# Kernel tuning notes

Measured on AMD Instinct MI355X. Metric: run time of the kernel, lower is better.

## Reference

```python
import jax, jax.numpy as jnp
import numpy as np

B, C, H, W = 4, 256, 64, 64
NUM_HEADS, HIDDEN = 2, 64


def setup_inputs() -> dict:
    key = jax.random.key(0)
    k1, k2, k3 = jax.random.split(key, 3)
    x = jax.random.normal(k1, (B, C, H, W), dtype=jnp.float32)
    # per-head fused QKV 1x1 conv weights: [num_heads, 3*hidden, C]
    embed_w = jax.random.normal(k2, (NUM_HEADS, 3 * HIDDEN, C), dtype=jnp.float32) * (2.0 / C) ** 0.5
    embed_b = jnp.zeros((NUM_HEADS, 3 * HIDDEN), dtype=jnp.float32)
    # output ConvTranspose2d kernel-1 weight: [in=hidden*heads, out=C]
    out_w = jax.random.normal(k3, (HIDDEN * NUM_HEADS, C), dtype=jnp.float32) * (2.0 / C) ** 0.5
    out_b = jnp.zeros((C,), dtype=jnp.float32)
    return {"x": x, "embed_w": embed_w, "embed_b": embed_b, "out_w": out_w, "out_b": out_b}


def reference(x, embed_w, embed_b, out_w, out_b):
    b, c, h, w = x.shape
    n = h * w
    scale = c ** (-0.5)  # scaled=True uses in_channels**-0.5
    xf = x.reshape(b, c, n)  # [B,C,N]
    # fused QKV projection for all heads (1x1 conv == channel matmul)
    qkv = jnp.einsum('bcn,hdc->bhdn', xf, embed_w) + embed_b[None, :, :, None]  # [B,Hh,3*hc,N]
    q, k, v = jnp.split(qkv, 3, axis=2)  # each [B,Hh,hc,N]
    # attention over flattened spatial positions
    attn = jax.nn.softmax(jnp.einsum('bhcm,bhcn->bhmn', q, k) * scale, axis=-1)  # [B,Hh,N,N]
    o = jnp.einsum('bhmn,bhcn->bhcm', attn, v)  # [B,Hh,hc,N]
    o = o.reshape(b, -1, n)  # concat heads -> [B, hc*Hh, N]
    # output 1x1 transpose conv: sum over input channel dim d of weight[d, c]
    out = jnp.einsum('bdn,dc->bcn', o, out_w) + out_b[None, :, None]
    out = out.reshape(b, c, h, w)
    return out + x  # residual=True
```

## Files before the change

kernel.cpp:

```cpp
#include <hip/hip_runtime.h>

#define B_SZ  4
#define C_IN  256
#define N_POS 4096
#define NH    2
#define HC    64

typedef __attribute__((ext_vector_type(8))) __bf16 bf16x8;
typedef __attribute__((ext_vector_type(4))) float  f32x4;
typedef unsigned short u16;

__device__ __forceinline__ u16 f2bf(float f) {
  unsigned u = __float_as_uint(f);
  u = u + 0x7FFF + ((u >> 16) & 1);
  return (u16)(u >> 16);
}

#if __has_builtin(__builtin_amdgcn_exp2f)
  #define EXP2(x) __builtin_amdgcn_exp2f(x)
#else
  #define EXP2(x) exp2f(x)
#endif

__device__ __forceinline__ unsigned cvtpk_bf16(float lo, float hi) {
  unsigned r;
  asm("v_cvt_pk_bf16_f32 %0, %1, %2" : "=v"(r) : "v"(lo), "v"(hi));
  return r;
}

__device__ __forceinline__ void gload_lds16(const void* g, void* l) {
  __builtin_amdgcn_global_load_lds(
      (const __attribute__((address_space(1))) unsigned*)g,
      (__attribute__((address_space(3))) unsigned*)l, 16, 0, 0);
}

__global__ __launch_bounds__(256) void k_prep_x(const float* __restrict__ x,
                                                u16* __restrict__ xt) {
  __shared__ float tile[32][33];
  int b = blockIdx.z, c0 = blockIdx.y * 32, n0 = blockIdx.x * 32;
  int tx = threadIdx.x, ty = threadIdx.y;
  const float* src = x + ((size_t)b * C_IN + c0) * N_POS + n0;
#pragma unroll
  for (int i = 0; i < 4; i++) tile[ty + 8*i][tx] = src[(size_t)(ty + 8*i) * N_POS + tx];
  __syncthreads();
  u16* dst = xt + ((size_t)b * N_POS + n0) * C_IN + c0;
#pragma unroll
  for (int i = 0; i < 4; i++) dst[(size_t)(ty + 8*i) * C_IN + tx] = f2bf(tile[tx][ty + 8*i]);
}

__global__ __launch_bounds__(256) void k_prep_w(const float* __restrict__ ew,
                                                const float* __restrict__ ow,
                                                u16* __restrict__ wbf,
                                                u16* __restrict__ w2t) {
  int i = blockIdx.x * 256 + threadIdx.x;
  if (i < 384 * 256) wbf[i] = f2bf(ew[i]);
  if (i < 128 * 256) {
    int d = i >> 8, c = i & 255;
    w2t[c * 128 + d] = f2bf(ow[i]);
  }
}

__global__ __launch_bounds__(256) void k_qkv(const u16* __restrict__ xt,
                                             const u16* __restrict__ wbf,
                                             const float* __restrict__ eb,
                                             u16* __restrict__ Qt,
                                             u16* __restrict__ Kt,
                                             u16* __restrict__ Vs) {
  int b = blockIdx.z;
  int mt = blockIdx.y;
  int nt = blockIdx.x;
  int w = threadIdx.x >> 6, l = threadIdx.x & 63;
  int lr = l & 15, lg = l >> 4;
  int h = mt / 3, type = mt % 3;

  const u16* arow = xt + ((size_t)b * N_POS + nt*64 + w*16 + lr) * C_IN + lg*8;
  const u16* brow = wbf + ((size_t)(mt*64) + lr) * C_IN + lg*8;

  f32x4 acc[4] = {};
#pragma unroll
  for (int kk = 0; kk < 8; kk++) {
    bf16x8 a = *(const bf16x8*)(arow + kk*32);
#pragma unroll
    for (int mf = 0; mf < 4; mf++) {
      bf16x8 bf = *(const bf16x8*)(brow + (size_t)mf*16*C_IN + kk*32);
      acc[mf] = __builtin_amdgcn_mfma_f32_16x16x32_bf16(a, bf, acc[mf], 0, 0, 0);
    }
  }

  const float QSCALE = 0.0625f * 1.44269504088896f;
  int bh = b * NH + h;
  int n0 = nt*64 + w*16 + lg*4;
#pragma unroll
  for (int mf = 0; mf < 4; mf++) {
    int cl = mf*16 + lr;
    float bias = eb[h*192 + type*64 + cl];
    if (type == 0) {
      u16* q = Qt + (size_t)bh * N_POS * HC;
#pragma unroll
      for (int r = 0; r < 4; r++) q[(size_t)(n0+r)*HC + cl] = f2bf((acc[mf][r] + bias) * QSCALE);
    } else if (type == 1) {
      u16* kd = Kt + (size_t)bh * N_POS * HC;
#pragma unroll
      for (int r = 0; r < 4; r++) kd[(size_t)(n0+r)*HC + cl] = f2bf(acc[mf][r] + bias);
    } else {
      u16* vd = Vs + (size_t)bh * (N_POS * HC);
      size_t idx = ((((size_t)nt*2 + (w>>1))*4 + lg)*64 + cl)*8 + 4*(w&1);
      ushort4 pk;
      pk.x = f2bf(acc[mf][0] + bias);
      pk.y = f2bf(acc[mf][1] + bias);
      pk.z = f2bf(acc[mf][2] + bias);
      pk.w = f2bf(acc[mf][3] + bias);
      *(ushort4*)(vd + idx) = pk;
    }
  }
}

__device__ __forceinline__ void softmax_tile(f32x4 (&s)[4], f32x4& psv, float& rm,
                                             f32x4 (&o)[4]) {
  float mx = s[0][0];
#pragma unroll
  for (int nf = 0; nf < 4; nf++)
#pragma unroll
    for (int r = 0; r < 4; r++) mx = fmaxf(mx, s[nf][r]);
  mx = fmaxf(mx, __shfl_xor(mx, 16));
  mx = fmaxf(mx, __shfl_xor(mx, 32));
  float nm = fmaxf(rm, mx);
  float corr = EXP2(rm - nm);
  rm = nm;
#pragma unroll
  for (int r = 0; r < 4; r++) psv[r] *= corr;
#pragma unroll
  for (int nf = 0; nf < 4; nf++)
#pragma unroll
    for (int r = 0; r < 4; r++) {
      float p = EXP2(s[nf][r] - nm);
      s[nf][r] = p;
      psv[r] += p;
    }
#pragma unroll
  for (int cf = 0; cf < 4; cf++)
#pragma unroll
    for (int r = 0; r < 4; r++) o[cf][r] *= corr;
}

__global__ __launch_bounds__(1024, 4) void k_attn(const u16* __restrict__ Qt,
                                                  const u16* __restrict__ Kt,
                                                  const u16* __restrict__ Vs,
                                                  u16* __restrict__ Ot) {
  int id = blockIdx.x;
  int bh = id & 7;
  int mt = id >> 3;
  int b = bh >> 1, h = bh & 1;
  int tid = threadIdx.x;
  int wid = tid >> 6;
  int l = tid & 63, lr = l & 15, lg = l >> 4;
  int qi = wid & 3;
  int ci = wid >> 2;
  int m0 = mt*128 + qi*32;

  __shared__ __align__(16) char smem[131072];
  __shared__ float Lps[4][8][16];
  __shared__ float Lm[4][8][16];

  bf16x8 qf[2][2];
#pragma unroll
  for (int sub = 0; sub < 2; sub++) {
    const u16* qb = Qt + ((size_t)bh * N_POS + m0 + sub*16 + lr) * HC + lg*8;
    qf[sub][0] = *(const bf16x8*)qb;
    qf[sub][1] = *(const bf16x8*)(qb + 32);
  }

  const char* Kt_bh = (const char*)(Kt + (size_t)bh * N_POS * HC);
  const char* Vs_bh = (const char*)(Vs + (size_t)bh * N_POS * HC);
  int gtid = tid & 255;

  f32x4 o0[4] = {}, o1[4] = {};
  f32x4 ps0 = {}, ps1 = {};
  float rm0 = -1e30f, rm1 = -1e30f;
  int xr = (lr & 7) << 4;

  union PF { bf16x8 v; unsigned u[4]; };

  auto stage = [&](int tile, char* sb) {
    const char* ksrc = Kt_bh + (size_t)tile * 8192;
    const char* vsrc = Vs_bh + (size_t)tile * 8192;
#pragma unroll
    for (int j = 0; j < 2; j++) {
      int off = (j*256 + gtid) * 16;
      int koff = off ^ (((off >> 7) & 7) << 4);
      gload_lds16(ksrc + koff, sb + off);
      gload_lds16(vsrc + off, sb + 8192 + off);
    }
  };

  stage(ci*16, smem + ci*16384);
  __syncthreads();

  int buf = 0;
  for (int t = 0; t < 16; t++) {
    if (t < 15) stage(ci*16 + t + 1, smem + (buf^1)*65536 + ci*16384);

    const char* Kb = smem + buf*65536 + ci*16384;
    const char* Vb = Kb + 8192;

    f32x4 s0[4], s1[4];
#pragma unroll
    for (int nf = 0; nf < 4; nf++) {
      const char* kr = Kb + (nf*16 + lr) * 128;
      bf16x8 k0 = *(const bf16x8*)(kr + ((lg*16)      ^ xr));
      bf16x8 k1 = *(const bf16x8*)(kr + ((lg*16 + 64) ^ xr));
      f32x4 z0 = {}, z1 = {};
      z0 = __builtin_amdgcn_mfma_f32_16x16x32_bf16(k0, qf[0][0], z0, 0, 0, 0);
      s0[nf] = __builtin_amdgcn_mfma_f32_16x16x32_bf16(k1, qf[0][1], z0, 0, 0, 0);
      z1 = __builtin_amdgcn_mfma_f32_16x16x32_bf16(k0, qf[1][0], z1, 0, 0, 0);
      s1[nf] = __builtin_amdgcn_mfma_f32_16x16x32_bf16(k1, qf[1][1], z1, 0, 0, 0);
    }

    softmax_tile(s0, ps0, rm0, o0);
    softmax_tile(s1, ps1, rm1, o1);

#pragma unroll
    for (int kk = 0; kk < 2; kk++) {
      PF pa, pb;
      pa.u[0] = cvtpk_bf16(s0[2*kk+0][0], s0[2*kk+0][1]);
      pa.u[1] = cvtpk_bf16(s0[2*kk+0][2], s0[2*kk+0][3]);
      pa.u[2] = cvtpk_bf16(s0[2*kk+1][0], s0[2*kk+1][1]);
      pa.u[3] = cvtpk_bf16(s0[2*kk+1][2], s0[2*kk+1][3]);
      pb.u[0] = cvtpk_bf16(s1[2*kk+0][0], s1[2*kk+0][1]);
      pb.u[1] = cvtpk_bf16(s1[2*kk+0][2], s1[2*kk+0][3]);
      pb.u[2] = cvtpk_bf16(s1[2*kk+1][0], s1[2*kk+1][1]);
      pb.u[3] = cvtpk_bf16(s1[2*kk+1][2], s1[2*kk+1][3]);
#pragma unroll
      for (int cf = 0; cf < 4; cf++) {
        bf16x8 vf = *(const bf16x8*)(Vb + (kk*4 + lg)*1024 + (cf*16 + lr)*16);
        o0[cf] = __builtin_amdgcn_mfma_f32_16x16x32_bf16(vf, pa.v, o0[cf], 0, 0, 0);
        o1[cf] = __builtin_amdgcn_mfma_f32_16x16x32_bf16(vf, pb.v, o1[cf], 0, 0, 0);
      }
    }

    __syncthreads();
    buf ^= 1;
  }

  float psa = ps0[0] + ps0[1] + ps0[2] + ps0[3];
  psa += __shfl_xor(psa, 16);
  psa += __shfl_xor(psa, 32);
  float psb = ps1[0] + ps1[1] + ps1[2] + ps1[3];
  psb += __shfl_xor(psb, 16);
  psb += __shfl_xor(psb, 32);

  float (*Lo)[8][16][64] = (float (*)[8][16][64])smem;
#pragma unroll
  for (int cf = 0; cf < 4; cf++) {
    *(f32x4*)&Lo[ci][qi*2+0][lr][cf*16 + 4*lg] = o0[cf];
    *(f32x4*)&Lo[ci][qi*2+1][lr][cf*16 + 4*lg] = o1[cf];
  }
  if (lg == 0) {
    Lps[ci][qi*2+0][lr] = psa; Lm[ci][qi*2+0][lr] = rm0;
    Lps[ci][qi*2+1][lr] = psb; Lm[ci][qi*2+1][lr] = rm1;
  }
  __syncthreads();

  int row = tid >> 3;
  int c0 = (tid & 7) * 8;
  int g = row >> 4, r2 = row & 15;
  float m0_ = Lm[0][g][r2], m1_ = Lm[1][g][r2];
  float m2_ = Lm[2][g][r2], m3_ = Lm[3][g][r2];
  float M = fmaxf(fmaxf(m0_, m1_), fmaxf(m2_, m3_));
  float w0 = EXP2(m0_ - M), w1 = EXP2(m1_ - M);
  float w2 = EXP2(m2_ - M), w3 = EXP2(m3_ - M);
  f32x4 accA, accB;
  {
    f32x4 a0 = *(const f32x4*)&Lo[0][g][r2][c0];
    f32x4 a1 = *(const f32x4*)&Lo[1][g][r2][c0];
    f32x4 a2 = *(const f32x4*)&Lo[2][g][r2][c0];
    f32x4 a3 = *(const f32x4*)&Lo[3][g][r2][c0];
#pragma unroll
    for (int i = 0; i < 4; i++) accA[i] = a0[i]*w0 + a1[i]*w1 + a2[i]*w2 + a3[i]*w3;
    f32x4 b0 = *(const f32x4*)&Lo[0][g][r2][c0+4];
    f32x4 b1 = *(const f32x4*)&Lo[1][g][r2][c0+4];
    f32x4 b2 = *(const f32x4*)&Lo[2][g][r2][c0+4];
    f32x4 b3 = *(const f32x4*)&Lo[3][g][r2][c0+4];
#pragma unroll
    for (int i = 0; i < 4; i++) accB[i] = b0[i]*w0 + b1[i]*w1 + b2[i]*w2 + b3[i]*w3;
  }
  float pst = Lps[0][g][r2]*w0 + Lps[1][g][r2]*w1
            + Lps[2][g][r2]*w2 + Lps[3][g][r2]*w3;
  float rinv = 1.0f / pst;
  u16* ob = Ot + ((size_t)b * N_POS + mt*128 + row) * (NH*HC) + h*HC + c0;
  uint4 st;
  st.x = cvtpk_bf16(accA[0]*rinv, accA[1]*rinv);
  st.y = cvtpk_bf16(accA[2]*rinv, accA[3]*rinv);
  st.z = cvtpk_bf16(accB[0]*rinv, accB[1]*rinv);
  st.w = cvtpk_bf16(accB[2]*rinv, accB[3]*rinv);
  *(uint4*)ob = st;
}

__global__ __launch_bounds__(256) void k_out(const u16* __restrict__ Ot,
                                             const u16* __restrict__ w2t,
                                             const float* __restrict__ obias,
                                             const float* __restrict__ x,
                                             float* __restrict__ out) {
  int b = blockIdx.z;
  int ct = blockIdx.y;
  int nt = blockIdx.x;
  int w = threadIdx.x >> 6, l = threadIdx.x & 63;
  int lr = l & 15, lg = l >> 4;

  const u16* arow = Ot + ((size_t)b * N_POS + nt*64 + w*16 + lr) * 128 + lg*8;
  const u16* brow = w2t + ((size_t)(ct*64) + lr) * 128 + lg*8;

  f32x4 acc[4] = {};
#pragma unroll
  for (int kk = 0; kk < 4; kk++) {
    bf16x8 a = *(const bf16x8*)(arow + kk*32);
#pragma unroll
    for (int cf = 0; cf < 4; cf++) {
      bf16x8 bf = *(const bf16x8*)(brow + (size_t)cf*16*128 + kk*32);
      acc[cf] = __builtin_amdgcn_mfma_f32_16x16x32_bf16(a, bf, acc[cf], 0, 0, 0);
    }
  }

  int n0 = nt*64 + w*16 + lg*4;
#pragma unroll
  for (int cf = 0; cf < 4; cf++) {
    int c = ct*64 + cf*16 + lr;
    float bias = obias[c];
    const float* xp = x + ((size_t)b * C_IN + c) * N_POS + n0;
    float* op = out + ((size_t)b * C_IN + c) * N_POS + n0;
    f32x4 xv = *(const f32x4*)xp;
    f32x4 rv;
#pragma unroll
    for (int i = 0; i < 4; i++) rv[i] = acc[cf][i] + bias + xv[i];
    *(f32x4*)op = rv;
  }
}

extern "C" void kernel_launch(void* const* d_in, const int* in_sizes, int n_in,
                              void* d_out, int out_size, void* d_ws, size_t ws_size,
                              hipStream_t stream) {
  const float* x  = (const float*)d_in[0];
  const float* ew = (const float*)d_in[1];
  const float* eb = (const float*)d_in[2];
  const float* ow = (const float*)d_in[3];
  const float* ob = (const float*)d_in[4];
  float* out = (float*)d_out;

  char* ws = (char*)d_ws;
  u16* xt  = (u16*)(ws + 0);
  u16* wbf = (u16*)(ws + 8388608);
  u16* w2t = (u16*)(ws + 8585216);
  u16* Qt  = (u16*)(ws + 8650752);
  u16* Kt  = (u16*)(ws + 12845056);
  u16* Vs  = (u16*)(ws + 17039360);
  u16* Ot  = (u16*)(ws + 21233664);

  hipLaunchKernelGGL(k_prep_x, dim3(128, 8, 4), dim3(32, 8), 0, stream, x, xt);
  hipLaunchKernelGGL(k_prep_w, dim3(384), dim3(256), 0, stream, ew, ow, wbf, w2t);
  hipLaunchKernelGGL(k_qkv,  dim3(64, 6, 4), dim3(256), 0, stream, xt, wbf, eb, Qt, Kt, Vs);
  hipLaunchKernelGGL(k_attn, dim3(256),      dim3(1024), 0, stream, Qt, Kt, Vs, Ot);
  hipLaunchKernelGGL(k_out,  dim3(64, 4, 4), dim3(256), 0, stream, Ot, w2t, ob, x, out);
}
```

Measured before the change: 105.9 us.

## Halve attention block size, single-buffer KV, swizzle LDS reduction, remap QKV grid

The attention kernel drops from 1024-thread blocks covering 128 query rows to 512-thread blocks covering 64 rows, and launches twice as many blocks. K/V staging becomes single-buffered with an extra barrier, which halves LDS per block so more blocks can share a CU, but loads no longer overlap compute within a block. MFMA sections are wrapped in s_setprio. The cross-wave reduction buffer gets a rotated column layout to avoid LDS bank conflicts. The QKV projection uses a 1D grid whose low bits pick (batch, head) so that work is spread across XCDs.

```diff
diff --git a/kernel.cpp b/kernel.cpp
--- a/kernel.cpp
+++ b/kernel.cpp
@@ -66,12 +66,16 @@
                                              u16* __restrict__ Qt,
                                              u16* __restrict__ Kt,
                                              u16* __restrict__ Vs) {
-  int b = blockIdx.z;
-  int mt = blockIdx.y;
-  int nt = blockIdx.x;
+  int id = blockIdx.x;
+  int xcd = id & 7;
+  int b = xcd >> 1, half = xcd & 1;
+  int rest = id >> 3;
+  int type = rest % 3;
+  int nt = rest / 3;
+  int mt = half*3 + type;
+  int h = half;
   int w = threadIdx.x >> 6, l = threadIdx.x & 63;
   int lr = l & 15, lg = l >> 4;
-  int h = mt / 3, type = mt % 3;
 
   const u16* arow = xt + ((size_t)b * N_POS + nt*64 + w*16 + lr) * C_IN + lg*8;
   const u16* brow = wbf + ((size_t)(mt*64) + lr) * C_IN + lg*8;
@@ -143,10 +147,10 @@
     for (int r = 0; r < 4; r++) o[cf][r] *= corr;
 }
 
-__global__ __launch_bounds__(1024, 4) void k_attn(const u16* __restrict__ Qt,
-                                                  const u16* __restrict__ Kt,
-                                                  const u16* __restrict__ Vs,
-                                                  u16* __restrict__ Ot) {
+__global__ __launch_bounds__(512, 4) void k_attn(const u16* __restrict__ Qt,
+                                                 const u16* __restrict__ Kt,
+                                                 const u16* __restrict__ Vs,
+                                                 u16* __restrict__ Ot) {
   int id = blockIdx.x;
   int bh = id & 7;
   int mt = id >> 3;
@@ -154,13 +158,13 @@
   int tid = threadIdx.x;
   int wid = tid >> 6;
   int l = tid & 63, lr = l & 15, lg = l >> 4;
-  int qi = wid & 3;
-  int ci = wid >> 2;
-  int m0 = mt*128 + qi*32;
-
-  __shared__ __align__(16) char smem[131072];
-  __shared__ float Lps[4][8][16];
-  __shared__ float Lm[4][8][16];
+  int qi = wid & 1;
+  int ci = wid >> 1;
+  int m0 = mt*64 + qi*32;
+
+  __shared__ __align__(16) char smem[65536];
+  __shared__ float Lps[4][4][16];
+  __shared__ float Lm[4][4][16];
 
   bf16x8 qf[2][2];
 #pragma unroll
@@ -172,7 +176,7 @@
 
   const char* Kt_bh = (const char*)(Kt + (size_t)bh * N_POS * HC);
   const char* Vs_bh = (const char*)(Vs + (size_t)bh * N_POS * HC);
-  int gtid = tid & 255;
+  int gtid = tid & 127;
 
   f32x4 o0[4] = {}, o1[4] = {};
   f32x4 ps0 = {}, ps1 = {};
@@ -181,29 +185,28 @@
 
   union PF { bf16x8 v; unsigned u[4]; };
 
-  auto stage = [&](int tile, char* sb) {
+  auto stage = [&](int tile) {
     const char* ksrc = Kt_bh + (size_t)tile * 8192;
     const char* vsrc = Vs_bh + (size_t)tile * 8192;
-#pragma unroll
-    for (int j = 0; j < 2; j++) {
-      int off = (j*256 + gtid) * 16;
+    char* sb = smem + ci*16384;
+#pragma unroll
+    for (int j = 0; j < 4; j++) {
+      int off = (j*128 + gtid) * 16;
       int koff = off ^ (((off >> 7) & 7) << 4);
       gload_lds16(ksrc + koff, sb + off);
       gload_lds16(vsrc + off, sb + 8192 + off);
     }
   };
 
-  stage(ci*16, smem + ci*16384);
+  stage(ci*16);
   __syncthreads();
 
-  int buf = 0;
   for (int t = 0; t < 16; t++) {
-    if (t < 15) stage(ci*16 + t + 1, smem + (buf^1)*65536 + ci*16384);
-
-    const char* Kb = smem + buf*65536 + ci*16384;
+    const char* Kb = smem + ci*16384;
     const char* Vb = Kb + 8192;
 
     f32x4 s0[4], s1[4];
+    __builtin_amdgcn_s_setprio(1);
 #pragma unroll
     for (int nf = 0; nf < 4; nf++) {
       const char* kr = Kb + (nf*16 + lr) * 128;
@@ -215,10 +218,12 @@
       z1 = __builtin_amdgcn_mfma_f32_16x16x32_bf16(k0, qf[1][0], z1, 0, 0, 0);
       s1[nf] = __builtin_amdgcn_mfma_f32_16x16x32_bf16(k1, qf[1][1], z1, 0, 0, 0);
     }
+    __builtin_amdgcn_s_setprio(0);
 
     softmax_tile(s0, ps0, rm0, o0);
     softmax_tile(s1, ps1, rm1, o1);
 
+    __builtin_amdgcn_s_setprio(1);
 #pragma unroll
     for (int kk = 0; kk < 2; kk++) {
       PF pa, pb;
@@ -237,9 +242,11 @@
         o1[cf] = __builtin_amdgcn_mfma_f32_16x16x32_bf16(vf, pb.v, o1[cf], 0, 0, 0);
       }
     }
+    __builtin_amdgcn_s_setprio(0);
 
     __syncthreads();
-    buf ^= 1;
+    if (t < 15) stage(ci*16 + t + 1);
+    __syncthreads();
   }
 
   float psa = ps0[0] + ps0[1] + ps0[2] + ps0[3];
@@ -249,11 +256,12 @@
   psb += __shfl_xor(psb, 16);
   psb += __shfl_xor(psb, 32);
 
-  float (*Lo)[8][16][64] = (float (*)[8][16][64])smem;
+  float (*Lo)[4][16][64] = (float (*)[4][16][64])smem;
 #pragma unroll
   for (int cf = 0; cf < 4; cf++) {
-    *(f32x4*)&Lo[ci][qi*2+0][lr][cf*16 + 4*lg] = o0[cf];
-    *(f32x4*)&Lo[ci][qi*2+1][lr][cf*16 + 4*lg] = o1[cf];
+    int colw = ((cf*16 + 4*lg) + 4*lr) & 63;
+    *(f32x4*)&Lo[ci][qi*2+0][lr][colw] = o0[cf];
+    *(f32x4*)&Lo[ci][qi*2+1][lr][colw] = o1[cf];
   }
   if (lg == 0) {
     Lps[ci][qi*2+0][lr] = psa; Lm[ci][qi*2+0][lr] = rm0;
@@ -269,25 +277,27 @@
   float M = fmaxf(fmaxf(m0_, m1_), fmaxf(m2_, m3_));
   float w0 = EXP2(m0_ - M), w1 = EXP2(m1_ - M);
   float w2 = EXP2(m2_ - M), w3 = EXP2(m3_ - M);
+  int ca = (c0 + 4*r2) & 63;
+  int cb = (c0 + 4 + 4*r2) & 63;
   f32x4 accA, accB;
   {
-    f32x4 a0 = *(const f32x4*)&Lo[0][g][r2][c0];
-    f32x4 a1 = *(const f32x4*)&Lo[1][g][r2][c0];
-    f32x4 a2 = *(const f32x4*)&Lo[2][g][r2][c0];
-    f32x4 a3 = *(const f32x4*)&Lo[3][g][r2][c0];
+    f32x4 a0 = *(const f32x4*)&Lo[0][g][r2][ca];
+    f32x4 a1 = *(const f32x4*)&Lo[1][g][r2][ca];
+    f32x4 a2 = *(const f32x4*)&Lo[2][g][r2][ca];
+    f32x4 a3 = *(const f32x4*)&Lo[3][g][r2][ca];
 #pragma unroll
     for (int i = 0; i < 4; i++) accA[i] = a0[i]*w0 + a1[i]*w1 + a2[i]*w2 + a3[i]*w3;
-    f32x4 b0 = *(const f32x4*)&Lo[0][g][r2][c0+4];
-    f32x4 b1 = *(const f32x4*)&Lo[1][g][r2][c0+4];
-    f32x4 b2 = *(const f32x4*)&Lo[2][g][r2][c0+4];
-    f32x4 b3 = *(const f32x4*)&Lo[3][g][r2][c0+4];
+    f32x4 b0 = *(const f32x4*)&Lo[0][g][r2][cb];
+    f32x4 b1 = *(const f32x4*)&Lo[1][g][r2][cb];
+    f32x4 b2 = *(const f32x4*)&Lo[2][g][r2][cb];
+    f32x4 b3 = *(const f32x4*)&Lo[3][g][r2][cb];
 #pragma unroll
     for (int i = 0; i < 4; i++) accB[i] = b0[i]*w0 + b1[i]*w1 + b2[i]*w2 + b3[i]*w3;
   }
   float pst = Lps[0][g][r2]*w0 + Lps[1][g][r2]*w1
             + Lps[2][g][r2]*w2 + Lps[3][g][r2]*w3;
   float rinv = 1.0f / pst;
-  u16* ob = Ot + ((size_t)b * N_POS + mt*128 + row) * (NH*HC) + h*HC + c0;
+  u16* ob = Ot + ((size_t)b * N_POS + mt*64 + row) * (NH*HC) + h*HC + c0;
   uint4 st;
   st.x = cvtpk_bf16(accA[0]*rinv, accA[1]*rinv);
   st.y = cvtpk_bf16(accA[2]*rinv, accA[3]*rinv);
@@ -357,7 +367,7 @@
 
   hipLaunchKernelGGL(k_prep_x, dim3(128, 8, 4), dim3(32, 8), 0, stream, x, xt);
   hipLaunchKernelGGL(k_prep_w, dim3(384), dim3(256), 0, stream, ew, ow, wbf, w2t);
-  hipLaunchKernelGGL(k_qkv,  dim3(64, 6, 4), dim3(256), 0, stream, xt, wbf, eb, Qt, Kt, Vs);
-  hipLaunchKernelGGL(k_attn, dim3(256),      dim3(1024), 0, stream, Qt, Kt, Vs, Ot);
+  hipLaunchKernelGGL(k_qkv,  dim3(1536),     dim3(256), 0, stream, xt, wbf, eb, Qt, Kt, Vs);
+  hipLaunchKernelGGL(k_attn, dim3(512),      dim3(512), 0, stream, Qt, Kt, Vs, Ot);
   hipLaunchKernelGGL(k_out,  dim3(64, 4, 4), dim3(256), 0, stream, Ot, w2t, ob, x, out);
 }
```

Measured after the change: 107.2 us. About the same (+1.2%).

## Fuse x transpose/bf16 cast into QKV GEMM, add MFMA priority and LDS swizzle

Applied to the files above, without the earlier changes.

Removes the separate k_prep_x kernel. The QKV kernel now loads fp32 x directly, converts it to bf16 and stages a swizzled 64x256 tile in LDS. Each block computes all 192 output channels of one head for 64 positions, so x is read once per head instead of once per Q/K/V type. This drops a kernel launch and the round trip of the intermediate xt buffer, at the cost of 32KB of LDS per block and more accumulators per thread. The attention kernel also raises wave priority around its MFMA sections and rotates columns in the output-merge LDS buffer to reduce bank conflicts.

```diff
diff --git a/kernel.cpp b/kernel.cpp
--- a/kernel.cpp
+++ b/kernel.cpp
@@ -32,20 +32,6 @@
   __builtin_amdgcn_global_load_lds(
       (const __attribute__((address_space(1))) unsigned*)g,
       (__attribute__((address_space(3))) unsigned*)l, 16, 0, 0);
-}
-
-__global__ __launch_bounds__(256) void k_prep_x(const float* __restrict__ x,
-                                                u16* __restrict__ xt) {
-  __shared__ float tile[32][33];
-  int b = blockIdx.z, c0 = blockIdx.y * 32, n0 = blockIdx.x * 32;
-  int tx = threadIdx.x, ty = threadIdx.y;
-  const float* src = x + ((size_t)b * C_IN + c0) * N_POS + n0;
-#pragma unroll
-  for (int i = 0; i < 4; i++) tile[ty + 8*i][tx] = src[(size_t)(ty + 8*i) * N_POS + tx];
-  __syncthreads();
-  u16* dst = xt + ((size_t)b * N_POS + n0) * C_IN + c0;
-#pragma unroll
-  for (int i = 0; i < 4; i++) dst[(size_t)(ty + 8*i) * C_IN + tx] = f2bf(tile[tx][ty + 8*i]);
 }
 
 __global__ __launch_bounds__(256) void k_prep_w(const float* __restrict__ ew,
@@ -60,57 +46,91 @@
   }
 }
 
-__global__ __launch_bounds__(256) void k_qkv(const u16* __restrict__ xt,
+__global__ __launch_bounds__(256) void k_qkv(const float* __restrict__ x,
                                              const u16* __restrict__ wbf,
                                              const float* __restrict__ eb,
                                              u16* __restrict__ Qt,
                                              u16* __restrict__ Kt,
                                              u16* __restrict__ Vs) {
-  int b = blockIdx.z;
-  int mt = blockIdx.y;
-  int nt = blockIdx.x;
-  int w = threadIdx.x >> 6, l = threadIdx.x & 63;
-  int lr = l & 15, lg = l >> 4;
-  int h = mt / 3, type = mt % 3;
-
-  const u16* arow = xt + ((size_t)b * N_POS + nt*64 + w*16 + lr) * C_IN + lg*8;
-  const u16* brow = wbf + ((size_t)(mt*64) + lr) * C_IN + lg*8;
-
-  f32x4 acc[4] = {};
+  int id = blockIdx.x;
+  int xcd = id & 7;
+  int b = xcd >> 1, h = xcd & 1;
+  int nt = id >> 3;
+  int tid = threadIdx.x;
+  int w = tid >> 6, l = tid & 63, lr = l & 15, lg = l >> 4;
+
+  __shared__ __align__(16) u16 Xl[64 * 256];
+
+  const float* xb = x + (size_t)b * C_IN * N_POS + nt*64;
+  {
+    int n = l;
+#pragma unroll
+    for (int pass = 0; pass < 8; pass++) {
+      int oct = w + pass*4;
+      int cb8 = oct * 8;
+      float v[8];
+#pragma unroll
+      for (int j = 0; j < 8; j++) v[j] = xb[(size_t)(cb8 + j) * N_POS + n];
+      union { bf16x8 vv; unsigned u[4]; } pk;
+#pragma unroll
+      for (int jj = 0; jj < 4; jj++) pk.u[jj] = cvtpk_bf16(v[2*jj], v[2*jj+1]);
+      int slot = oct ^ ((n & 7) << 2);
+      *(bf16x8*)&Xl[n * 256 + slot * 8] = pk.vv;
+    }
+  }
+  __syncthreads();
+
+  f32x4 acc[4][3] = {};
+  const u16* brow[3];
+#pragma unroll
+  for (int i = 0; i < 3; i++)
+    brow[i] = wbf + (size_t)(h*192 + (3*w + i)*16 + lr) * C_IN + lg*8;
+
 #pragma unroll
   for (int kk = 0; kk < 8; kk++) {
-    bf16x8 a = *(const bf16x8*)(arow + kk*32);
-#pragma unroll
-    for (int mf = 0; mf < 4; mf++) {
-      bf16x8 bf = *(const bf16x8*)(brow + (size_t)mf*16*C_IN + kk*32);
-      acc[mf] = __builtin_amdgcn_mfma_f32_16x16x32_bf16(a, bf, acc[mf], 0, 0, 0);
+    bf16x8 bfr[3];
+#pragma unroll
+    for (int i = 0; i < 3; i++) bfr[i] = *(const bf16x8*)(brow[i] + kk*32);
+#pragma unroll
+    for (int nsub = 0; nsub < 4; nsub++) {
+      int n2 = nsub*16 + lr;
+      int sp = (kk*4 + lg) ^ ((lr & 7) << 2);
+      bf16x8 a = *(const bf16x8*)&Xl[n2*256 + sp*8];
+#pragma unroll
+      for (int i = 0; i < 3; i++)
+        acc[nsub][i] = __builtin_amdgcn_mfma_f32_16x16x32_bf16(a, bfr[i], acc[nsub][i], 0, 0, 0);
     }
   }
 
   const float QSCALE = 0.0625f * 1.44269504088896f;
   int bh = b * NH + h;
-  int n0 = nt*64 + w*16 + lg*4;
-#pragma unroll
-  for (int mf = 0; mf < 4; mf++) {
+#pragma unroll
+  for (int i = 0; i < 3; i++) {
+    int s3 = 3*w + i;
+    int type = s3 >> 2, mf = s3 & 3;
     int cl = mf*16 + lr;
     float bias = eb[h*192 + type*64 + cl];
-    if (type == 0) {
-      u16* q = Qt + (size_t)bh * N_POS * HC;
-#pragma unroll
-      for (int r = 0; r < 4; r++) q[(size_t)(n0+r)*HC + cl] = f2bf((acc[mf][r] + bias) * QSCALE);
-    } else if (type == 1) {
-      u16* kd = Kt + (size_t)bh * N_POS * HC;
-#pragma unroll
-      for (int r = 0; r < 4; r++) kd[(size_t)(n0+r)*HC + cl] = f2bf(acc[mf][r] + bias);
-    } else {
-      u16* vd = Vs + (size_t)bh * (N_POS * HC);
-      size_t idx = ((((size_t)nt*2 + (w>>1))*4 + lg)*64 + cl)*8 + 4*(w&1);
-      ushort4 pk;
-      pk.x = f2bf(acc[mf][0] + bias);
-      pk.y = f2bf(acc[mf][1] + bias);
-      pk.z = f2bf(acc[mf][2] + bias);
-      pk.w = f2bf(acc[mf][3] + bias);
-      *(ushort4*)(vd + idx) = pk;
+#pragma unroll
+    for (int nsub = 0; nsub < 4; nsub++) {
+      int n0 = nt*64 + nsub*16 + lg*4;
+      if (type == 0) {
+        u16* q = Qt + (size_t)bh * N_POS * HC;
+#pragma unroll
+        for (int r = 0; r < 4; r++) q[(size_t)(n0+r)*HC + cl] = f2bf((acc[nsub][i][r] + bias) * QSCALE);
+      } else if (type == 1) {
+        u16* kd = Kt + (size_t)bh * N_POS * HC;
+#pragma unroll
+        for (int r = 0; r < 4; r++) kd[(size_t)(n0+r)*HC + cl] = f2bf(acc[nsub][i][r] + bias);
+      } else {
+        u16* vd = Vs + (size_t)bh * (N_POS * HC);
+        size_t idx = ((((size_t)nt*2 + (nsub>>1))*4 + lg)*64 + cl)*8 + 4*(nsub&1);
+        ushort4 pk;
+        pk.x = f2bf(acc[nsub][i][0] + bias);
+        pk.y = f2bf(acc[nsub][i][1] + bias);
+        pk.z = f2bf(acc[nsub][i][2] + bias);
+        pk.w = f2bf(acc[nsub][i][3] + bias);
+        *(ushort4*)(vd + idx) = pk;
+      }
     }
   }
 }
@@ -204,6 +224,7 @@
     const char* Vb = Kb + 8192;
 
     f32x4 s0[4], s1[4];
+    __builtin_amdgcn_s_setprio(1);
 #pragma unroll
     for (int nf = 0; nf < 4; nf++) {
       const char* kr = Kb + (nf*16 + lr) * 128;
@@ -215,10 +236,12 @@
       z1 = __builtin_amdgcn_mfma_f32_16x16x32_bf16(k0, qf[1][0], z1, 0, 0, 0);
       s1[nf] = __builtin_amdgcn_mfma_f32_16x16x32_bf16(k1, qf[1][1], z1, 0, 0, 0);
     }
+    __builtin_amdgcn_s_setprio(0);
 
     softmax_tile(s0, ps0, rm0, o0);
     softmax_tile(s1, ps1, rm1, o1);
 
+    __builtin_amdgcn_s_setprio(1);
 #pragma unroll
     for (int kk = 0; kk < 2; kk++) {
       PF pa, pb;
@@ -237,6 +260,7 @@
         o1[cf] = __builtin_amdgcn_mfma_f32_16x16x32_bf16(vf, pb.v, o1[cf], 0, 0, 0);
       }
     }
+    __builtin_amdgcn_s_setprio(0);
 
     __syncthreads();
     buf ^= 1;
@@ -252,8 +276,9 @@
   float (*Lo)[8][16][64] = (float (*)[8][16][64])smem;
 #pragma unroll
   for (int cf = 0; cf < 4; cf++) {
-    *(f32x4*)&Lo[ci][qi*2+0][lr][cf*16 + 4*lg] = o0[cf];
-    *(f32x4*)&Lo[ci][qi*2+1][lr][cf*16 + 4*lg] = o1[cf];
+    int colw = ((cf*16 + 4*lg) + 4*lr) & 63;
+    *(f32x4*)&Lo[ci][qi*2+0][lr][colw] = o0[cf];
+    *(f32x4*)&Lo[ci][qi*2+1][lr][colw] = o1[cf];
   }
   if (lg == 0) {
     Lps[ci][qi*2+0][lr] = psa; Lm[ci][qi*2+0][lr] = rm0;
@@ -269,18 +294,20 @@
   float M = fmaxf(fmaxf(m0_, m1_), fmaxf(m2_, m3_));
   float w0 = EXP2(m0_ - M), w1 = EXP2(m1_ - M);
   float w2 = EXP2(m2_ - M), w3 = EXP2(m3_ - M);
+  int ca = (c0 + 4*r2) & 63;
+  int cb = (c0 + 4 + 4*r2) & 63;
   f32x4 accA, accB;
   {
-    f32x4 a0 = *(const f32x4*)&Lo[0][g][r2][c0];
-    f32x4 a1 = *(const f32x4*)&Lo[1][g][r2][c0];
-    f32x4 a2 = *(const f32x4*)&Lo[2][g][r2][c0];
-    f32x4 a3 = *(const f32x4*)&Lo[3][g][r2][c0];
+    f32x4 a0 = *(const f32x4*)&Lo[0][g][r2][ca];
+    f32x4 a1 = *(const f32x4*)&Lo[1][g][r2][ca];
+    f32x4 a2 = *(const f32x4*)&Lo[2][g][r2][ca];
+    f32x4 a3 = *(const f32x4*)&Lo[3][g][r2][ca];
 #pragma unroll
     for (int i = 0; i < 4; i++) accA[i] = a0[i]*w0 + a1[i]*w1 + a2[i]*w2 + a3[i]*w3;
-    f32x4 b0 = *(const f32x4*)&Lo[0][g][r2][c0+4];
-    f32x4 b1 = *(const f32x4*)&Lo[1][g][r2][c0+4];
-    f32x4 b2 = *(const f32x4*)&Lo[2][g][r2][c0+4];
-    f32x4 b3 = *(const f32x4*)&Lo[3][g][r2][c0+4];
+    f32x4 b0 = *(const f32x4*)&Lo[0][g][r2][cb];
+    f32x4 b1 = *(const f32x4*)&Lo[1][g][r2][cb];
+    f32x4 b2 = *(const f32x4*)&Lo[2][g][r2][cb];
+    f32x4 b3 = *(const f32x4*)&Lo[3][g][r2][cb];
 #pragma unroll
     for (int i = 0; i < 4; i++) accB[i] = b0[i]*w0 + b1[i]*w1 + b2[i]*w2 + b3[i]*w3;
   }
@@ -347,17 +374,15 @@
   float* out = (float*)d_out;
 
   char* ws = (char*)d_ws;
-  u16* xt  = (u16*)(ws + 0);
-  u16* wbf = (u16*)(ws + 8388608);
-  u16* w2t = (u16*)(ws + 8585216);
-  u16* Qt  = (u16*)(ws + 8650752);
-  u16* Kt  = (u16*)(ws + 12845056);
-  u16* Vs  = (u16*)(ws + 17039360);
-  u16* Ot  = (u16*)(ws + 21233664);
-
-  hipLaunchKernelGGL(k_prep_x, dim3(128, 8, 4), dim3(32, 8), 0, stream, x, xt);
+  u16* wbf = (u16*)(ws + 0);
+  u16* w2t = (u16*)(ws + 196608);
+  u16* Qt  = (u16*)(ws + 262144);
+  u16* Kt  = (u16*)(ws + 4456448);
+  u16* Vs  = (u16*)(ws + 8650752);
+  u16* Ot  = (u16*)(ws + 12845056);
+
   hipLaunchKernelGGL(k_prep_w, dim3(384), dim3(256), 0, stream, ew, ow, wbf, w2t);
-  hipLaunchKernelGGL(k_qkv,  dim3(64, 6, 4), dim3(256), 0, stream, xt, wbf, eb, Qt, Kt, Vs);
+  hipLaunchKernelGGL(k_qkv,  dim3(512),      dim3(256), 0, stream, x, wbf, eb, Qt, Kt, Vs);
   hipLaunchKernelGGL(k_attn, dim3(256),      dim3(1024), 0, stream, Qt, Kt, Vs, Ot);
   hipLaunchKernelGGL(k_out,  dim3(64, 4, 4), dim3(256), 0, stream, Ot, w2t, ob, x, out);
 }
```

Measured after the change: 88.31 us, median of 2. 1.2x faster.
